# Optimization experiments

Measured on AMD Instinct MI355X. Metric: run time of the kernel, lower is better.

## Reference

```python
import jax, jax.numpy as jnp
import numpy as np

SIGMA = 64.0      # diffusion kernel bandwidth (init kwarg sigma)
THRESH = 0.2      # edge threshold (init kwarg threshold)
J = 3             # number of wavelet scales (init kwarg J)
EPS = 1e-8


def setup_inputs() -> dict:
    key = jax.random.key(0)
    k1, k2 = jax.random.split(key)
    point_clouds = jax.random.normal(k1, (8, 1024, 32), dtype=jnp.float32)
    mask = jnp.ones((8, 1024), dtype=bool)
    alphas = jax.random.uniform(k2, (4, 32), dtype=jnp.float32)  # learned param
    return {"point_clouds": point_clouds, "mask": mask, "alphas": alphas}


def _diffusion(point_clouds, alphas, mask):
    """compute_diffusion_matrix: (B,nw,N,N) column-normalized diffusion + reweighted clouds."""
    d = point_clouds.shape[-1]
    # normalize_alphas=True branch
    a = jnp.sqrt(jnp.asarray(d, point_clouds.dtype)) * alphas / jnp.linalg.norm(alphas, axis=1, keepdims=True)
    Xb = point_clouds[:, None, :, :] * a[None, :, None, :]          # (B,nw,N,d)
    G = jnp.einsum('bwnd,bwmd->bwnm', Xb, Xb)                       # Gram
    dg = jnp.diagonal(G, axis1=-2, axis2=-1)                        # ||x||^2
    D = dg[..., None, :] + dg[..., :, None] - 2.0 * G               # pairwise sq dist
    W = jnp.exp(-D / SIGMA)
    W = jnp.where(W < THRESH, 0.0, W)
    pm = mask[:, None, :, None] & mask[:, None, None, :]
    W = jnp.where(pm, W, 0.0)
    deg = jnp.clip(W.sum(axis=2, keepdims=True), EPS)               # column sums (axis 2, as in torch)
    W = W / deg
    N = W.shape[-1]
    W = W + 0.5 * jnp.eye(N, dtype=W.dtype)                         # diagonal += 0.5
    return W, Xb


def _wavelet_features(W, Xb, mask):
    """Diffusion wavelet scattering: X, P^{2^J}X, |P^{2^{j-1}}X - P^{2^j}X|, masked mean pool."""
    scales = []                      # scales[j] = P^{2^j} X for j=0..J
    cur = jnp.einsum('bwnm,bwmd->bwnd', W, Xb)
    scales.append(cur)
    steps = 1
    for j in range(1, J + 1):
        target = 2 ** j
        while steps < target:
            cur = jnp.einsum('bwnm,bwmd->bwnd', W, cur)
            steps += 1
        scales.append(cur)
    wavelets = [jnp.abs(scales[j - 1] - scales[j]) for j in range(1, J + 1)]
    F = jnp.concatenate([Xb, scales[J]] + wavelets, axis=-1)        # (B,nw,N,(2+J)*d)
    m = mask[:, None, :, None].astype(F.dtype)
    pooled = (F * m).sum(axis=2) / jnp.clip(m.sum(axis=2), EPS)     # (B,nw,(2+J)*d)
    return pooled.reshape(pooled.shape[0], -1)                      # (B, nw*(2+J)*d)


def reference(point_clouds, mask, alphas):
    W, Xb = _diffusion(point_clouds, alphas, mask)
    return _wavelet_features(W, Xb, mask)
```

## Files before the change

### kernel.cpp

```cpp
#include <hip/hip_runtime.h>
#include <math.h>
#include <stdint.h>

#define N 1024
#define D 32
#define NPAIR 32

typedef _Float16 half8_t __attribute__((ext_vector_type(8)));
typedef _Float16 half4_t __attribute__((ext_vector_type(4)));
typedef float    f32x4   __attribute__((ext_vector_type(4)));
typedef long long i64;

#define WBLK8 16384
#define WPAIR ((size_t)1 << 20)
#define BARSTRIDE 32

__global__ __launch_bounds__(256) void k_xb(const float* __restrict__ pc,
                                            const float* __restrict__ alphas,
                                            float* __restrict__ sq,
                                            _Float16* __restrict__ xb16,
                                            _Float16* __restrict__ xb_t,
                                            float* __restrict__ out,
                                            int* __restrict__ bar) {
    int tid = threadIdx.x;
    int t = blockIdx.x * 256 + tid;
    if (t < 5120) out[t] = 0.f;
    if (t < 8192) bar[t] = 0;
    int p     = blockIdx.x >> 2;
    int nbase = (blockIdx.x & 3) * 256;
    int n     = nbase + tid;
    int b = p >> 2, w = p & 3;
    const float* src = pc + ((size_t)(b * 1024 + n)) * 32;
    const float* aw  = alphas + w * 32;
    float s2a = 0.f;
#pragma unroll
    for (int k = 0; k < 32; ++k) { float av = aw[k]; s2a = fmaf(av, av, s2a); }
    float scale = sqrtf(32.0f) / sqrtf(s2a);

    __shared__ _Float16 lds[32][264];
    _Float16* rowp = xb16 + ((size_t)p * 1024 + n) * 32;
    _Float16 h[32];
    float s = 0.f;
#pragma unroll
    for (int k = 0; k < 32; k += 4) {
        float4 v  = *(const float4*)(src + k);
        float4 av = *(const float4*)(aw + k);
        h[k]     = (_Float16)(v.x * av.x * scale);
        h[k + 1] = (_Float16)(v.y * av.y * scale);
        h[k + 2] = (_Float16)(v.z * av.z * scale);
        h[k + 3] = (_Float16)(v.w * av.w * scale);
#pragma unroll
        for (int j = 0; j < 4; ++j) {
            float f = (float)h[k + j];
            s = fmaf(f, f, s);
            lds[k + j][tid] = h[k + j];
        }
    }
#pragma unroll
    for (int k = 0; k < 32; k += 8) *(half8_t*)(rowp + k) = *(half8_t*)(h + k);
    sq[p * N + n] = s;
    __syncthreads();
    {
        int f = tid >> 3, c = tid & 7;
        _Float16* dst = xb_t + (size_t)p * 32 * N + (size_t)f * N + nbase + c * 32;
#pragma unroll
        for (int j = 0; j < 4; ++j)
            *(half8_t*)(dst + j * 8) = *(const half8_t*)(&lds[f][c * 32 + j * 8]);
    }
}

#define BIN_PITCH 1032

__device__ __forceinline__ void stage_bin_cs(_Float16 (*bin)[BIN_PITCH],
                                             float* csum,
                                             const _Float16* __restrict__ binG,
                                             int p) {
    int t = threadIdx.x;
    int f = t >> 4, seg = t & 15;
    const _Float16* src = binG + (size_t)p * 32 * N + (size_t)f * 1024 + seg * 8;
    half8_t v[8];
#pragma unroll
    for (int j = 0; j < 8; ++j) v[j] = *(const half8_t*)(src + j * 128);
    float ps = 0.f;
#pragma unroll
    for (int j = 0; j < 8; ++j) {
        *(half8_t*)(&bin[f][(seg + j * 16) * 8]) = v[j];
#pragma unroll
        for (int k = 0; k < 8; ++k) ps += (float)v[j][k];
    }
    ps += __shfl_xor(ps, 1);
    ps += __shfl_xor(ps, 2);
    ps += __shfl_xor(ps, 4);
    ps += __shfl_xor(ps, 8);
    if (seg == 0) csum[f] = ps;
    __syncthreads();
}

__device__ __forceinline__ half8_t unpack_w(uint2 a8) {
    const uint32_t kExp = 0x64646464u;
    union { uint32_t u[4]; half8_t h; } o;
    o.u[0] = __builtin_amdgcn_perm(a8.x, kExp, 0x00050004u);
    o.u[1] = __builtin_amdgcn_perm(a8.x, kExp, 0x00070006u);
    o.u[2] = __builtin_amdgcn_perm(a8.y, kExp, 0x00050004u);
    o.u[3] = __builtin_amdgcn_perm(a8.y, kExp, 0x00070006u);
    return o.h;
}

__device__ __forceinline__ void preload_w(const uint8_t* __restrict__ W8,
                                          int p, int rowblk, int lane,
                                          uint2* wreg) {
    const uint8_t* aptr = W8 + (size_t)p * WPAIR + (size_t)rowblk * WBLK8 + lane * 8;
#pragma unroll
    for (int kt = 0; kt < 32; ++kt)
        wreg[kt] = *(const uint2*)(aptr + kt * 512);
}

__device__ __forceinline__ void apply_core_reg(const uint2* wreg,
                                               const _Float16 (*bin)[BIN_PITCH],
                                               int lane,
                                               f32x4& acc0, f32x4& acc1) {
    int r    = lane & 15;
    int quad = lane >> 4;
    acc0 = (f32x4){0.f, 0.f, 0.f, 0.f};
    acc1 = (f32x4){0.f, 0.f, 0.f, 0.f};
#pragma unroll
    for (int kt = 0; kt < 32; ++kt) {
        half8_t a  = unpack_w(wreg[kt]);
        half8_t b0 = *(const half8_t*)(&bin[r][kt * 32 + quad * 8]);
        half8_t b1 = *(const half8_t*)(&bin[r + 16][kt * 32 + quad * 8]);
        acc0 = __builtin_amdgcn_mfma_f32_16x16x32_f16(a, b0, acc0, 0, 0, 0);
        acc1 = __builtin_amdgcn_mfma_f32_16x16x32_f16(a, b1, acc1, 0, 0, 0);
    }
}

__device__ __forceinline__ void pair_barrier(int* __restrict__ bar, int slot) {
    __syncthreads();
    if (threadIdx.x == 0) {
        int* ctr = bar + slot * BARSTRIDE;
        __hip_atomic_fetch_add(ctr, 1, __ATOMIC_RELAXED, __HIP_MEMORY_SCOPE_AGENT);
        for (int spin = 0; spin < 1600000; ++spin) {
            if (__hip_atomic_load(ctr, __ATOMIC_RELAXED,
                                  __HIP_MEMORY_SCOPE_AGENT) >= 8) break;
            __builtin_amdgcn_s_sleep(1);
        }
    }
    __syncthreads();
}

__global__ __launch_bounds__(512) void k_fused(const _Float16* __restrict__ xb16,
                                               const float* __restrict__ sq,
                                               const _Float16* __restrict__ xb_t,
                                               uint8_t* __restrict__ W8,
                                               _Float16* __restrict__ rdeg16,
                                               _Float16* __restrict__ bb,
                                               int* __restrict__ bar,
                                               float* __restrict__ out) {
    const size_t HOP = (size_t)NPAIR * 32 * N;
    int phys = blockIdx.x;
    int xcd  = phys & 7;
    int i    = phys >> 3;
    int p    = xcd * 4 + (i >> 3);
    int mt8  = i & 7;
    int wv8  = threadIdx.x >> 6;
    int lane = threadIdx.x & 63;
    int r    = lane & 15;
    int quad = lane >> 4;

    __shared__ char lds_raw[32 * BIN_PITCH * 2];
    __shared__ float csum[32];
    __shared__ uint8_t tbuf8[8][16][80];
    __shared__ int     cred[8][64];
    __shared__ float   rloc[2][64];
    _Float16 (*bin)[BIN_PITCH] = (_Float16 (*)[BIN_PITCH])lds_raw;

    {
        int tid256 = threadIdx.x & 255;
        int half   = threadIdx.x >> 8;
        int m0     = (mt8 * 2 + half) * 64;
        int wvg    = tid256 >> 6;

        const _Float16* xp = xb16 + (size_t)p * N * D;
        const float*   sqp = sq + p * N;
        uint8_t*       Wp8 = W8 + (size_t)p * WPAIR;

        half8_t bfr[4];
        float sqm[4];
#pragma unroll
        for (int t = 0; t < 4; ++t) {
            bfr[t] = *(const half8_t*)(xp + (size_t)(m0 + t * 16 + r) * 32 + quad * 8);
            sqm[t] = sqp[m0 + t * 16 + r];
        }
        int colacc[4] = {0, 0, 0, 0};

        for (int rg = 0; rg < 16; ++rg) {
            int n0w = rg * 64 + wvg * 16;
            half8_t afr = *(const half8_t*)(xp + (size_t)(n0w + r) * 32 + quad * 8);
            float4 sqn = *(const float4*)(sqp + n0w + quad * 4);
#pragma unroll
            for (int t = 0; t < 4; ++t) {
                f32x4 g = {0.f, 0.f, 0.f, 0.f};
                g = __builtin_amdgcn_mfma_f32_16x16x32_f16(afr, bfr[t], g, 0, 0, 0);
                float sn[4] = {sqn.x, sqn.y, sqn.z, sqn.w};
#pragma unroll
                for (int gi = 0; gi < 4; ++gi) {
                    float Dv = sn[gi] + sqm[t] - 2.f * g[gi];
                    float wvv = __expf(Dv * (-1.0f / 64.0f));
                    wvv = (wvv >= 0.2f) ? wvv : 0.f;
                    int q = (int)__builtin_rintf(wvv * 127.0f);
                    colacc[t] += q;
                    tbuf8[wv8][quad * 4 + gi][t * 16 + r] = (uint8_t)q;
                }
            }
            int rowblk = rg * 4 + wvg;
#pragma unroll
            for (int ktl = 0; ktl < 2; ++ktl) {
                i64 v = *(const i64*)(&tbuf8[wv8][r][ktl * 32 + quad * 8]);
                *(i64*)(Wp8 + (size_t)rowblk * WBLK8
                            + (size_t)((m0 >> 5) + ktl) * 512 + lane * 8) = v;
            }
        }
#pragma unroll
        for (int t = 0; t < 4; ++t) {
            colacc[t] += __shfl_xor(colacc[t], 16);
            colacc[t] += __shfl_xor(colacc[t], 32);
        }
        if (quad == 0) {
#pragma unroll
            for (int t = 0; t < 4; ++t) cred[wv8][t * 16 + r] = colacc[t];
        }
        __syncthreads();
        if (tid256 < 64) {
            int hb = half * 4;
            int s = cred[hb][tid256] + cred[hb + 1][tid256]
                  + cred[hb + 2][tid256] + cred[hb + 3][tid256];
            _Float16 rd = (_Float16)(127.0f / fmaxf((float)s, 1.0f));
            rdeg16[p * N + m0 + tid256] = rd;
            rloc[half][tid256] = (float)rd;
        }
        __syncthreads();
        {
            int f   = tid256 >> 3;
            int s8i = tid256 & 7;
            const _Float16* xt = xb_t + (size_t)p * 32 * N + (size_t)f * N
                               + m0 + s8i * 8;
            half8_t v = *(const half8_t*)xt;
            half8_t bo;
#pragma unroll
            for (int j = 0; j < 8; ++j)
                bo[j] = (_Float16)((float)v[j] * rloc[half][s8i * 8 + j]);
            *(half8_t*)(bb + (size_t)p * 32 * N + (size_t)f * N + m0 + s8i * 8) = bo;
        }
    }

    pair_barrier(bar, 7 * 32 + p);

    int wv   = wv8;
    int n0   = mt8 * 128 + wv * 16;
    int rowblk = mt8 * 8 + wv;

    uint2 wreg[32];
    preload_w(W8, p, rowblk, lane, wreg);

#pragma unroll 1
    for (int h = 0; h < 7; ++h) {
        stage_bin_cs(bin, csum, bb + (size_t)h * HOP, p);
        f32x4 acc0, acc1;
        apply_core_reg(wreg, bin, lane, acc0, acc1);

        const float c = 1.0f / 127.0f;
        float corr0 = 1024.0f * csum[r];
        float corr1 = 1024.0f * csum[r + 16];
        half4_t rv  = *(const half4_t*)(rdeg16 + p * N + n0 + quad * 4);
        half4_t bc0 = *(const half4_t*)(&bin[r][n0 + quad * 4]);
        half4_t bc1 = *(const half4_t*)(&bin[r + 16][n0 + quad * 4]);
        half4_t ob0, ob1;
#pragma unroll
        for (int j = 0; j < 4; ++j) {
            float t0 = (acc0[j] - corr0) * c;
            float t1 = (acc1[j] - corr1) * c;
            ob0[j] = (_Float16)((float)rv[j] * t0 + 0.5f * (float)bc0[j]);
            ob1[j] = (_Float16)((float)rv[j] * t1 + 0.5f * (float)bc1[j]);
        }
        _Float16* obp = bb + (size_t)(h + 1) * HOP + (size_t)p * 32 * N;
        *(half4_t*)(obp + (size_t)r * N        + n0 + quad * 4) = ob0;
        *(half4_t*)(obp + (size_t)(r + 16) * N + n0 + quad * 4) = ob1;

        pair_barrier(bar, h * 32 + p);
    }

    stage_bin_cs(bin, csum, bb + (size_t)7 * HOP, p);
    f32x4 acc0, acc1;
    apply_core_reg(wreg, bin, lane, acc0, acc1);

    const float c = 1.0f / 127.0f;
    float corr0 = 1024.0f * csum[r];
    float corr1 = 1024.0f * csum[r + 16];
    half4_t rv  = *(const half4_t*)(rdeg16 + p * N + n0 + quad * 4);
    half4_t bc0 = *(const half4_t*)(&bin[r][n0 + quad * 4]);
    half4_t bc1 = *(const half4_t*)(&bin[r + 16][n0 + quad * 4]);
    float P80[4], P81[4];
#pragma unroll
    for (int j = 0; j < 4; ++j) {
        float ir = 1.0f / (float)rv[j];
        P80[j] = (acc0[j] - corr0) * c + 0.5f * (float)bc0[j] * ir;
        P81[j] = (acc1[j] - corr1) * c + 0.5f * (float)bc1[j] * ir;
    }
    __syncthreads();

    float (*pl)[33] = (float (*)[33])lds_raw;
    float* invr = (float*)(lds_raw + 128 * 33 * 4);
#pragma unroll
    for (int j = 0; j < 4; ++j) {
        pl[wv * 16 + quad * 4 + j][r]      = P80[j];
        pl[wv * 16 + quad * 4 + j][r + 16] = P81[j];
    }
    if (threadIdx.x < 128)
        invr[threadIdx.x] = 1.0f / (float)rdeg16[p * N + mt8 * 128 + threadIdx.x];
    __syncthreads();

    const _Float16* b1 = bb + 1 * HOP;
    const _Float16* b2 = bb + 2 * HOP;
    const _Float16* b4 = bb + 4 * HOP;
    int ch = threadIdx.x;
    if (ch < 160) {
        int g = ch >> 5, f = ch & 31;
        int n0blk = mt8 * 128;
        size_t base = (size_t)p * 32 * N + (size_t)f * N + n0blk;
        float s = 0.f;
        if (g == 0) {
#pragma unroll
            for (int it = 0; it < 16; ++it) {
                half8_t va = *(const half8_t*)(xb_t + base + it * 8);
#pragma unroll
                for (int j = 0; j < 8; ++j) s += (float)va[j];
            }
        } else if (g == 1) {
#pragma unroll
            for (int n = 0; n < 128; ++n) s += pl[n][f];
        } else if (g == 2) {
#pragma unroll
            for (int it = 0; it < 16; ++it) {
                half8_t va = *(const half8_t*)(b1 + base + it * 8);
                half8_t vb = *(const half8_t*)(b2 + base + it * 8);
#pragma unroll
                for (int j = 0; j < 8; ++j)
                    s += fabsf((float)va[j] - (float)vb[j]) * invr[it * 8 + j];
            }
        } else if (g == 3) {
#pragma unroll
            for (int it = 0; it < 16; ++it) {
                half8_t va = *(const half8_t*)(b2 + base + it * 8);
                half8_t vb = *(const half8_t*)(b4 + base + it * 8);
#pragma unroll
                for (int j = 0; j < 8; ++j)
                    s += fabsf((float)va[j] - (float)vb[j]) * invr[it * 8 + j];
            }
        } else {
#pragma unroll
            for (int it = 0; it < 16; ++it) {
                half8_t va = *(const half8_t*)(b4 + base + it * 8);
#pragma unroll
                for (int j = 0; j < 8; ++j)
                    s += fabsf((float)va[j] * invr[it * 8 + j] - pl[it * 8 + j][f]);
            }
        }
        int b = p >> 2, w = p & 3;
        atomicAdd(out + b * 640 + w * 160 + ch, s * (1.0f / 1024.0f));
    }
}

extern "C" void kernel_launch(void* const* d_in, const int* in_sizes, int n_in,
                              void* d_out, int out_size, void* d_ws, size_t ws_size,
                              hipStream_t stream) {
    const float* pc     = (const float*)d_in[0];
    const float* alphas = (const float*)d_in[2];
    float* out = (float*)d_out;
    char* ws = (char*)d_ws;

    float* sq = (float*)ws;                     ws += 32768 * 4;
    int* bar = (int*)ws;                        ws += 8192 * 4;
    _Float16* rdeg16 = (_Float16*)ws;           ws += 32768 * 2;
    uint8_t* W8 = (uint8_t*)ws;                 ws += (size_t)NPAIR * WPAIR;
    const size_t SB = (size_t)NPAIR * 32 * N * 2;
    _Float16* xb16 = (_Float16*)ws;             ws += SB;
    _Float16* xb_t = (_Float16*)ws;             ws += SB;
    _Float16* bb   = (_Float16*)ws;             ws += 8 * SB;

    k_xb   <<<dim3(128), dim3(256), 0, stream>>>(pc, alphas, sq, xb16, xb_t, out, bar);
    k_fused<<<dim3(256), dim3(512), 0, stream>>>(xb16, sq, xb_t, W8, rdeg16, bb, bar, out);
}
```

Measured before the change: 129.9 us.

## Build quantized W tiles directly in registers, exchange only column-sum partials

```diff
diff --git a/kernel.cpp b/kernel.cpp
--- a/kernel.cpp
+++ b/kernel.cpp
@@ -9,11 +9,9 @@
 typedef _Float16 half8_t __attribute__((ext_vector_type(8)));
 typedef _Float16 half4_t __attribute__((ext_vector_type(4)));
 typedef float    f32x4   __attribute__((ext_vector_type(4)));
-typedef long long i64;
-
-#define WBLK8 16384
-#define WPAIR ((size_t)1 << 20)
+
 #define BARSTRIDE 32
+#define BIN_PITCH 1032
 
 __global__ __launch_bounds__(256) void k_xb(const float* __restrict__ pc,
                                             const float* __restrict__ alphas,
@@ -69,8 +67,6 @@
     }
 }
 
-#define BIN_PITCH 1032
-
 __device__ __forceinline__ void stage_bin_cs(_Float16 (*bin)[BIN_PITCH],
                                              float* csum,
                                              const _Float16* __restrict__ binG,
@@ -106,15 +102,6 @@
     return o.h;
 }
 
-__device__ __forceinline__ void preload_w(const uint8_t* __restrict__ W8,
-                                          int p, int rowblk, int lane,
-                                          uint2* wreg) {
-    const uint8_t* aptr = W8 + (size_t)p * WPAIR + (size_t)rowblk * WBLK8 + lane * 8;
-#pragma unroll
-    for (int kt = 0; kt < 32; ++kt)
-        wreg[kt] = *(const uint2*)(aptr + kt * 512);
-}
-
 __device__ __forceinline__ void apply_core_reg(const uint2* wreg,
                                                const _Float16 (*bin)[BIN_PITCH],
                                                int lane,
@@ -150,8 +137,7 @@
 __global__ __launch_bounds__(512) void k_fused(const _Float16* __restrict__ xb16,
                                                const float* __restrict__ sq,
                                                const _Float16* __restrict__ xb_t,
-                                               uint8_t* __restrict__ W8,
-                                               _Float16* __restrict__ rdeg16,
+                                               int* __restrict__ gpart,
                                                _Float16* __restrict__ bb,
                                                int* __restrict__ bar,
                                                float* __restrict__ out) {
@@ -161,125 +147,116 @@
     int i    = phys >> 3;
     int p    = xcd * 4 + (i >> 3);
     int mt8  = i & 7;
-    int wv8  = threadIdx.x >> 6;
+    int wv   = threadIdx.x >> 6;
     int lane = threadIdx.x & 63;
     int r    = lane & 15;
     int quad = lane >> 4;
+    int n0   = mt8 * 128 + wv * 16;
 
     __shared__ char lds_raw[32 * BIN_PITCH * 2];
     __shared__ float csum[32];
-    __shared__ uint8_t tbuf8[8][16][80];
-    __shared__ int     cred[8][64];
-    __shared__ float   rloc[2][64];
+    __shared__ uint8_t tbw[8][16][40];
+    __shared__ int colpart[1024];
+    __shared__ float rdeg_all[1024];
     _Float16 (*bin)[BIN_PITCH] = (_Float16 (*)[BIN_PITCH])lds_raw;
 
+    colpart[threadIdx.x] = 0;
+    colpart[threadIdx.x + 512] = 0;
+
+    const _Float16* xp  = xb16 + (size_t)p * N * D;
+    const float*    sqp = sq + p * N;
+    half8_t afr = *(const half8_t*)(xp + (size_t)(n0 + r) * 32 + quad * 8);
+    float4 sq4 = *(const float4*)(sqp + n0 + quad * 4);
+    float sn[4] = {sq4.x, sq4.y, sq4.z, sq4.w};
+    __syncthreads();
+
+    uint2 wreg[32];
+#pragma unroll
+    for (int kt = 0; kt < 32; ++kt) {
+#pragma unroll
+        for (int s = 0; s < 2; ++s) {
+            int mt = kt * 2 + s;
+            half8_t bfr = *(const half8_t*)(xp + (size_t)(mt * 16 + r) * 32 + quad * 8);
+            float sqm = sqp[mt * 16 + r];
+            f32x4 g = {0.f, 0.f, 0.f, 0.f};
+            g = __builtin_amdgcn_mfma_f32_16x16x32_f16(afr, bfr, g, 0, 0, 0);
+            int cp = 0;
+#pragma unroll
+            for (int gi = 0; gi < 4; ++gi) {
+                float Dv = sn[gi] + sqm - 2.f * g[gi];
+                float wvv = __expf(Dv * (-1.0f / 64.0f));
+                wvv = (wvv >= 0.2f) ? wvv : 0.f;
+                int q = (int)__builtin_rintf(wvv * 127.0f);
+                cp += q;
+                tbw[wv][quad * 4 + gi][s * 16 + r] = (uint8_t)q;
+            }
+            cp += __shfl_xor(cp, 16);
+            cp += __shfl_xor(cp, 32);
+            if (quad == 0) atomicAdd(&colpart[mt * 16 + r], cp);
+        }
+        wreg[kt] = *(const uint2*)(&tbw[wv][r][quad * 8]);
+    }
+    __syncthreads();
     {
-        int tid256 = threadIdx.x & 255;
-        int half   = threadIdx.x >> 8;
-        int m0     = (mt8 * 2 + half) * 64;
-        int wvg    = tid256 >> 6;
-
-        const _Float16* xp = xb16 + (size_t)p * N * D;
-        const float*   sqp = sq + p * N;
-        uint8_t*       Wp8 = W8 + (size_t)p * WPAIR;
-
-        half8_t bfr[4];
-        float sqm[4];
-#pragma unroll
-        for (int t = 0; t < 4; ++t) {
-            bfr[t] = *(const half8_t*)(xp + (size_t)(m0 + t * 16 + r) * 32 + quad * 8);
-            sqm[t] = sqp[m0 + t * 16 + r];
-        }
-        int colacc[4] = {0, 0, 0, 0};
-
-        for (int rg = 0; rg < 16; ++rg) {
-            int n0w = rg * 64 + wvg * 16;
-            half8_t afr = *(const half8_t*)(xp + (size_t)(n0w + r) * 32 + quad * 8);
-            float4 sqn = *(const float4*)(sqp + n0w + quad * 4);
-#pragma unroll
-            for (int t = 0; t < 4; ++t) {
-                f32x4 g = {0.f, 0.f, 0.f, 0.f};
-                g = __builtin_amdgcn_mfma_f32_16x16x32_f16(afr, bfr[t], g, 0, 0, 0);
-                float sn[4] = {sqn.x, sqn.y, sqn.z, sqn.w};
-#pragma unroll
-                for (int gi = 0; gi < 4; ++gi) {
-                    float Dv = sn[gi] + sqm[t] - 2.f * g[gi];
-                    float wvv = __expf(Dv * (-1.0f / 64.0f));
-                    wvv = (wvv >= 0.2f) ? wvv : 0.f;
-                    int q = (int)__builtin_rintf(wvv * 127.0f);
-                    colacc[t] += q;
-                    tbuf8[wv8][quad * 4 + gi][t * 16 + r] = (uint8_t)q;
-                }
-            }
-            int rowblk = rg * 4 + wvg;
-#pragma unroll
-            for (int ktl = 0; ktl < 2; ++ktl) {
-                i64 v = *(const i64*)(&tbuf8[wv8][r][ktl * 32 + quad * 8]);
-                *(i64*)(Wp8 + (size_t)rowblk * WBLK8
-                            + (size_t)((m0 >> 5) + ktl) * 512 + lane * 8) = v;
-            }
-        }
-#pragma unroll
-        for (int t = 0; t < 4; ++t) {
-            colacc[t] += __shfl_xor(colacc[t], 16);
-            colacc[t] += __shfl_xor(colacc[t], 32);
-        }
-        if (quad == 0) {
-#pragma unroll
-            for (int t = 0; t < 4; ++t) cred[wv8][t * 16 + r] = colacc[t];
-        }
-        __syncthreads();
-        if (tid256 < 64) {
-            int hb = half * 4;
-            int s = cred[hb][tid256] + cred[hb + 1][tid256]
-                  + cred[hb + 2][tid256] + cred[hb + 3][tid256];
-            _Float16 rd = (_Float16)(127.0f / fmaxf((float)s, 1.0f));
-            rdeg16[p * N + m0 + tid256] = rd;
-            rloc[half][tid256] = (float)rd;
-        }
-        __syncthreads();
-        {
-            int f   = tid256 >> 3;
-            int s8i = tid256 & 7;
-            const _Float16* xt = xb_t + (size_t)p * 32 * N + (size_t)f * N
-                               + m0 + s8i * 8;
-            half8_t v = *(const half8_t*)xt;
-            half8_t bo;
-#pragma unroll
-            for (int j = 0; j < 8; ++j)
-                bo[j] = (_Float16)((float)v[j] * rloc[half][s8i * 8 + j]);
-            *(half8_t*)(bb + (size_t)p * 32 * N + (size_t)f * N + m0 + s8i * 8) = bo;
-        }
-    }
-
+        int* gp = gpart + (size_t)(p * 8 + mt8) * 1024;
+        gp[threadIdx.x]       = colpart[threadIdx.x];
+        gp[threadIdx.x + 512] = colpart[threadIdx.x + 512];
+    }
     pair_barrier(bar, 7 * 32 + p);
 
-    int wv   = wv8;
-    int n0   = mt8 * 128 + wv * 16;
-    int rowblk = mt8 * 8 + wv;
-
-    uint2 wreg[32];
-    preload_w(W8, p, rowblk, lane, wreg);
-
+#pragma unroll
+    for (int c0 = 0; c0 < 2; ++c0) {
+        int c = threadIdx.x + c0 * 512;
+        int sdeg = 0;
+#pragma unroll
+        for (int b = 0; b < 8; ++b) sdeg += gpart[(size_t)(p * 8 + b) * 1024 + c];
+        rdeg_all[c] = (float)(_Float16)(127.0f / fmaxf((float)sdeg, 1.0f));
+    }
+    __syncthreads();
+
+    const float c = 1.0f / 127.0f;
 #pragma unroll 1
     for (int h = 0; h < 7; ++h) {
-        stage_bin_cs(bin, csum, bb + (size_t)h * HOP, p);
+        if (h == 0) {
+            int t = threadIdx.x, f = t >> 4, seg = t & 15;
+            const _Float16* src = xb_t + (size_t)p * 32 * N + (size_t)f * 1024 + seg * 8;
+            float ps = 0.f;
+#pragma unroll
+            for (int j = 0; j < 8; ++j) {
+                half8_t v = *(const half8_t*)(src + j * 128);
+                const float* rg = &rdeg_all[seg * 8 + j * 128];
+                half8_t bo;
+#pragma unroll
+                for (int k = 0; k < 8; ++k) {
+                    bo[k] = (_Float16)((float)v[k] * rg[k]);
+                    ps += (float)bo[k];
+                }
+                *(half8_t*)(&bin[f][(seg + j * 16) * 8]) = bo;
+            }
+            ps += __shfl_xor(ps, 1);
+            ps += __shfl_xor(ps, 2);
+            ps += __shfl_xor(ps, 4);
+            ps += __shfl_xor(ps, 8);
+            if (seg == 0) csum[f] = ps;
+            __syncthreads();
+        } else {
+            stage_bin_cs(bin, csum, bb + (size_t)h * HOP, p);
+        }
         f32x4 acc0, acc1;
         apply_core_reg(wreg, bin, lane, acc0, acc1);
 
-        const float c = 1.0f / 127.0f;
         float corr0 = 1024.0f * csum[r];
         float corr1 = 1024.0f * csum[r + 16];
-        half4_t rv  = *(const half4_t*)(rdeg16 + p * N + n0 + quad * 4);
         half4_t bc0 = *(const half4_t*)(&bin[r][n0 + quad * 4]);
         half4_t bc1 = *(const half4_t*)(&bin[r + 16][n0 + quad * 4]);
         half4_t ob0, ob1;
 #pragma unroll
         for (int j = 0; j < 4; ++j) {
+            float rvj = rdeg_all[n0 + quad * 4 + j];
             float t0 = (acc0[j] - corr0) * c;
             float t1 = (acc1[j] - corr1) * c;
-            ob0[j] = (_Float16)((float)rv[j] * t0 + 0.5f * (float)bc0[j]);
-            ob1[j] = (_Float16)((float)rv[j] * t1 + 0.5f * (float)bc1[j]);
+            ob0[j] = (_Float16)(rvj * t0 + 0.5f * (float)bc0[j]);
+            ob1[j] = (_Float16)(rvj * t1 + 0.5f * (float)bc1[j]);
         }
         _Float16* obp = bb + (size_t)(h + 1) * HOP + (size_t)p * 32 * N;
         *(half4_t*)(obp + (size_t)r * N        + n0 + quad * 4) = ob0;
@@ -292,16 +269,15 @@
     f32x4 acc0, acc1;
     apply_core_reg(wreg, bin, lane, acc0, acc1);
 
-    const float c = 1.0f / 127.0f;
     float corr0 = 1024.0f * csum[r];
     float corr1 = 1024.0f * csum[r + 16];
-    half4_t rv  = *(const half4_t*)(rdeg16 + p * N + n0 + quad * 4);
     half4_t bc0 = *(const half4_t*)(&bin[r][n0 + quad * 4]);
     half4_t bc1 = *(const half4_t*)(&bin[r + 16][n0 + quad * 4]);
     float P80[4], P81[4];
 #pragma unroll
     for (int j = 0; j < 4; ++j) {
-        float ir = 1.0f / (float)rv[j];
+        float rvj = rdeg_all[n0 + quad * 4 + j];
+        float ir = 1.0f / rvj;
         P80[j] = (acc0[j] - corr0) * c + 0.5f * (float)bc0[j] * ir;
         P81[j] = (acc1[j] - corr1) * c + 0.5f * (float)bc1[j] * ir;
     }
@@ -315,7 +291,7 @@
         pl[wv * 16 + quad * 4 + j][r + 16] = P81[j];
     }
     if (threadIdx.x < 128)
-        invr[threadIdx.x] = 1.0f / (float)rdeg16[p * N + mt8 * 128 + threadIdx.x];
+        invr[threadIdx.x] = 1.0f / rdeg_all[mt8 * 128 + threadIdx.x];
     __syncthreads();
 
     const _Float16* b1 = bb + 1 * HOP;
@@ -379,13 +355,12 @@
 
     float* sq = (float*)ws;                     ws += 32768 * 4;
     int* bar = (int*)ws;                        ws += 8192 * 4;
-    _Float16* rdeg16 = (_Float16*)ws;           ws += 32768 * 2;
-    uint8_t* W8 = (uint8_t*)ws;                 ws += (size_t)NPAIR * WPAIR;
+    int* gpart = (int*)ws;                      ws += 32 * 8 * 1024 * 4;
     const size_t SB = (size_t)NPAIR * 32 * N * 2;
     _Float16* xb16 = (_Float16*)ws;             ws += SB;
     _Float16* xb_t = (_Float16*)ws;             ws += SB;
     _Float16* bb   = (_Float16*)ws;             ws += 8 * SB;
 
     k_xb   <<<dim3(128), dim3(256), 0, stream>>>(pc, alphas, sq, xb16, xb_t, out, bar);
-    k_fused<<<dim3(256), dim3(512), 0, stream>>>(xb16, sq, xb_t, W8, rdeg16, bb, bar, out);
-}
+    k_fused<<<dim3(256), dim3(512), 0, stream>>>(xb16, sq, xb_t, gpart, bb, bar, out);
+}
```

Measured after the change: 127.1 us. -2.1%, faster.
